# Performance work log

Measured on AMD Instinct MI355X. Metric: run time of the kernel, lower is better.

The kernel has to match this reference:

```python
import jax, jax.numpy as jnp
import numpy as np

N = 50_000        # nodes
D = 256           # emb_dim
L = 3             # num_layer
E = 4             # num_experts (all hop-1 GCN experts)
K = 2             # top-k gating
VOCAB = 5000      # src_vocab_size_graph
NEDGES = 1_600_000
BN_EPS = 1e-5


def setup_inputs() -> dict:
    key = jax.random.key(0)
    ks = jax.random.split(key, 8)
    x = jax.random.randint(ks[0], (N,), 0, VOCAB)                      # atom ids
    edge_index = jax.random.randint(ks[1], (2, NEDGES), 0, N)          # [2, E_edges] src/dst
    emb = jax.random.normal(ks[2], (VOCAB + 1, D), jnp.float32) * 0.02 # AtomEncoder table
    w_gate = jax.random.normal(ks[3], (L, D, E), jnp.float32) * 0.02   # per-layer gate
    conv_W = jax.random.normal(ks[4], (L, E, D, D), jnp.float32) * (1.0 / np.sqrt(D))
    conv_b = jnp.zeros((L, E, D), jnp.float32)
    bn_gamma = jnp.ones((L, E, D), jnp.float32)
    bn_beta = jnp.zeros((L, E, D), jnp.float32)
    return dict(x=x, edge_index=edge_index, emb=emb, w_gate=w_gate,
                conv_W=conv_W, conv_b=conv_b, bn_gamma=bn_gamma, bn_beta=bn_beta)


def reference(x, edge_index, emb, w_gate, conv_W, conv_b, bn_gamma, bn_beta):
    src, dst = edge_index[0], edge_index[1]
    ones = jnp.ones((NEDGES,), jnp.float32)
    out_deg = jax.ops.segment_sum(ones, src, num_segments=N)
    in_deg = jax.ops.segment_sum(ones, dst, num_segments=N)
    norm_src = jax.lax.rsqrt(jnp.maximum(out_deg, 1.0))[:, None]  # D^{-1/2} on source side
    norm_dst = jax.lax.rsqrt(jnp.maximum(in_deg, 1.0))[:, None]   # D^{-1/2} on dest side

    h = emb[x]  # [N, D] AtomEncoder
    node_ids = jnp.arange(N)[:, None]
    for l in range(L):
        # ---- top-k sparse gating over experts ----
        logits = h @ w_gate[l]                              # [N, E]
        topv, topi = jax.lax.top_k(logits, K)               # [N, K]
        gk = jax.nn.softmax(topv, axis=-1)                  # renormalized top-k gates
        gates = jnp.zeros((N, E), h.dtype).at[node_ids, topi].set(gk)  # sparse [N, E]
        # ---- shared symmetric-normalized GCN aggregation (same A_norm for all experts) ----
        msg = (h * norm_src)[src]                           # [E_edges, D]
        agg = jax.ops.segment_sum(msg, dst, num_segments=N) * norm_dst  # [N, D]
        # ---- per-expert linear + BatchNorm (training-mode stats over nodes) ----
        z = jnp.einsum('nd,edf->enf', agg, conv_W[l]) + conv_b[l][:, None, :]  # [E, N, D]
        mu = z.mean(axis=1, keepdims=True)
        var = z.var(axis=1, keepdims=True)
        z = (z - mu) * jax.lax.rsqrt(var + BN_EPS) * bn_gamma[l][:, None, :] + bn_beta[l][:, None, :]
        # ---- combine with sparse gates (zero gates => expert math cancels) ----
        h_moe = jnp.einsum('ne,enf->nf', gates, z)          # [N, D]
        # outer residual: h = h + drop_path(relu(h)); drop_path is identity in eval
        h = h_moe + jax.nn.relu(h_moe)
    return h  # JK='last' node representation [N, D]
```

## Files before the change

### kernel.cpp

```cpp
#include <hip/hip_runtime.h>
#include <hip/hip_bf16.h>

#define N_NODES 50000
#define DIM     256
#define NEXP    4
#define NLAYER  3
#define NEDGE   1600000
#define BN_EPS  1e-5f

typedef __attribute__((ext_vector_type(8))) short          s16x8;
typedef __attribute__((ext_vector_type(8))) unsigned short u16x8;
typedef __attribute__((ext_vector_type(4))) float          f32x4;

static __device__ __forceinline__ float wave_reduce(float v) {
    #pragma unroll
    for (int off = 32; off; off >>= 1) v += __shfl_xor(v, off, 64);
    return v;
}

static __device__ __forceinline__ void bf16split(float x, unsigned short& hi,
                                                 unsigned short& lo) {
    unsigned xb = __float_as_uint(x);
    unsigned hb = (xb + 0x7FFFu + ((xb >> 16) & 1u)) & 0xFFFF0000u;
    float hif = __uint_as_float(hb);
    float l  = x - hif;
    unsigned lb2 = __float_as_uint(l);
    unsigned lb  = (lb2 + 0x7FFFu + ((lb2 >> 16) & 1u)) >> 16;
    hi = (unsigned short)(hb >> 16);
    lo = (unsigned short)lb;
}

__global__ void k_deg(const int* __restrict__ src, const int* __restrict__ dst,
                      int* __restrict__ cnt_out, int* __restrict__ cnt_in) {
    int i = blockIdx.x * 256 + threadIdx.x;
    if (i < NEDGE) {
        atomicAdd(&cnt_out[src[i]], 1);
        atomicAdd(&cnt_in[dst[i]], 1);
    }
}

__global__ void k_norm(const int* __restrict__ cnt_out, const int* __restrict__ cnt_in,
                       float* __restrict__ nsrc, float* __restrict__ ndst) {
    int i = blockIdx.x * 256 + threadIdx.x;
    if (i < N_NODES) {
        nsrc[i] = rsqrtf(fmaxf((float)cnt_out[i], 1.f));
        ndst[i] = rsqrtf(fmaxf((float)cnt_in[i], 1.f));
    }
}

__global__ __launch_bounds__(1024) void k_scan(const int* __restrict__ cnt_in,
                                               int* __restrict__ offs,
                                               int* __restrict__ cursor) {
    __shared__ int ps[1024];
    const int CH = 49;
    int t = threadIdx.x;
    int base = t * CH;
    int s = 0;
    for (int k = 0; k < CH; k++) { int i = base + k; if (i < N_NODES) s += cnt_in[i]; }
    ps[t] = s; __syncthreads();
    for (int off = 1; off < 1024; off <<= 1) {
        int v = ps[t];
        int u = (t >= off) ? ps[t - off] : 0;
        __syncthreads();
        ps[t] = v + u;
        __syncthreads();
    }
    int run = (t == 0) ? 0 : ps[t - 1];
    for (int k = 0; k < CH; k++) {
        int i = base + k;
        if (i < N_NODES) { offs[i] = run; cursor[i] = run; run += cnt_in[i]; }
    }
    if (t == 1023) offs[N_NODES] = ps[1023];
}

__global__ void k_fill(const int* __restrict__ src, const int* __restrict__ dst,
                       int* __restrict__ cursor, int* __restrict__ csr_s) {
    int i = blockIdx.x * 256 + threadIdx.x;
    if (i < NEDGE) {
        int s = src[i], d = dst[i];
        int pos = atomicAdd(&cursor[d], 1);
        csr_s[pos] = s;
    }
}

__global__ void k_emb(const int* __restrict__ x, const float4* __restrict__ emb4,
                      float4* __restrict__ h4) {
    int i = blockIdx.x * 256 + threadIdx.x;
    if (i < N_NODES * 64) {
        int n = i >> 6, c = i & 63;
        h4[i] = emb4[x[n] * 64 + c];
    }
}

__global__ void k_gate(const float4* __restrict__ h4, const float4* __restrict__ wg4,
                       int* __restrict__ pid, float* __restrict__ gaN,
                       float* __restrict__ gbN) {
    int n    = blockIdx.x * 4 + (threadIdx.x >> 6);
    int lane = threadIdx.x & 63;
    if (n >= N_NODES) return;
    float4 hv = h4[n * 64 + lane];
    const float* hp = (const float*)&hv;
    float4 acc = {0.f, 0.f, 0.f, 0.f};
    #pragma unroll
    for (int j = 0; j < 4; j++) {
        float4 w = wg4[lane * 4 + j];
        acc.x += hp[j] * w.x; acc.y += hp[j] * w.y;
        acc.z += hp[j] * w.z; acc.w += hp[j] * w.w;
    }
    acc.x = wave_reduce(acc.x); acc.y = wave_reduce(acc.y);
    acc.z = wave_reduce(acc.z); acc.w = wave_reduce(acc.w);
    if (lane == 0) {
        float lg[4] = {acc.x, acc.y, acc.z, acc.w};
        int e1 = 0;
        #pragma unroll
        for (int e = 1; e < 4; e++) if (lg[e] > lg[e1]) e1 = e;
        int e2 = -1;
        #pragma unroll
        for (int e = 0; e < 4; e++) {
            if (e == e1) continue;
            if (e2 < 0 || lg[e] > lg[e2]) e2 = e;
        }
        float v1 = lg[e1], v2 = lg[e2];
        float g2 = 1.f / (1.f + expf(v1 - v2));
        float g1 = 1.f - g2;
        int a = min(e1, e2), b = max(e1, e2);
        float ga = (e1 < e2) ? g1 : g2;
        float gb = (e1 < e2) ? g2 : g1;
        int p = (a == 0) ? (b - 1) : ((a == 1) ? (b + 1) : (b + 2));
        pid[n] = p; gaN[n] = ga; gbN[n] = gb;
    }
}

__global__ void k_bucket(const int* __restrict__ pid,
                         int* __restrict__ gcount, int* __restrict__ bnode) {
    __shared__ int cnt[6];
    __shared__ int basep[6];
    int t = threadIdx.x;
    int n = blockIdx.x * 256 + t;
    if (t < 6) cnt[t] = 0;
    __syncthreads();
    int p = 0, pos = 0;
    bool valid = (n < N_NODES);
    if (valid) { p = pid[n]; pos = atomicAdd(&cnt[p], 1); }
    __syncthreads();
    if (t < 6) basep[t] = atomicAdd(&gcount[t], cnt[t]);
    __syncthreads();
    if (valid) bnode[p * N_NODES + basep[p] + pos] = n;
}

__global__ void k_agg(const float4* __restrict__ h4,
                      const int* __restrict__ offs,
                      const int* __restrict__ csr_s, const float* __restrict__ nsrc,
                      const float* __restrict__ ndst,
                      float4* __restrict__ agg4) {
    const float S  = 4294967296.0f;
    const float SI = 1.0f / 4294967296.0f;
    int n    = blockIdx.x * 4 + (threadIdx.x >> 6);
    int lane = threadIdx.x & 63;
    if (n >= N_NODES) return;
    int beg = offs[n], end = offs[n + 1];
    long long ax = 0, ay = 0, az = 0, aw = 0;
    int j = beg;
    for (; j + 1 < end; j += 2) {
        int   s0 = csr_s[j],     s1 = csr_s[j + 1];
        float w0 = nsrc[s0] * S, w1 = nsrc[s1] * S;
        float4 a = h4[(size_t)s0 * 64 + lane];
        float4 b = h4[(size_t)s1 * 64 + lane];
        ax += (long long)(w0 * a.x) + (long long)(w1 * b.x);
        ay += (long long)(w0 * a.y) + (long long)(w1 * b.y);
        az += (long long)(w0 * a.z) + (long long)(w1 * b.z);
        aw += (long long)(w0 * a.w) + (long long)(w1 * b.w);
    }
    if (j < end) {
        int   s0 = csr_s[j];
        float w0 = nsrc[s0] * S;
        float4 a = h4[(size_t)s0 * 64 + lane];
        ax += (long long)(w0 * a.x); ay += (long long)(w0 * a.y);
        az += (long long)(w0 * a.z); aw += (long long)(w0 * a.w);
    }
    float nd = ndst[n] * SI;
    float4 o;
    o.x = nd * (float)ax; o.y = nd * (float)ay;
    o.z = nd * (float)az; o.w = nd * (float)aw;
    agg4[n * 64 + lane] = o;
}

__global__ void k_pcs(const float* __restrict__ agg,
                      unsigned short* __restrict__ Apk,
                      float* __restrict__ msum_p) {
    int t = threadIdx.x;
    const int CH = 200;
    int n0 = blockIdx.x * CH;
    float s = 0.f;
    for (int r = 0; r < CH; r++) {
        int n = n0 + r;
        float v = agg[(size_t)n * DIM + t];
        s += v;
        unsigned short hi, lo;
        bf16split(v, hi, lo);
        Apk[(size_t)n * 512 + t]       = hi;
        Apk[(size_t)n * 512 + 256 + t] = lo;
    }
    msum_p[blockIdx.x * 256 + t] = s;
}

#define GSL   48
#define GCH   1056
#define NPAIR 10
__global__ __launch_bounds__(256) void k_gram(const float* __restrict__ agg,
                                              float* __restrict__ Cp) {
    __shared__ float LA[16][64];
    __shared__ float LB[16][64];
    const int tiT[NPAIR] = {0,0,0,0,1,1,1,2,2,3};
    const int tjT[NPAIR] = {0,1,2,3,1,2,3,2,3,3};
    int t  = threadIdx.x;
    int sl = blockIdx.x;
    int pr = blockIdx.y;
    int ti = tiT[pr], tj = tjT[pr];
    int tx = t & 15, ty = t >> 4;
    float acc[4][4] = {};
    int nbase = sl * GCH;
    const float4* agg4 = (const float4*)agg;
    for (int s0 = 0; s0 < GCH; s0 += 16) {
        int r = ty;
        int n = nbase + s0 + r;
        float4 va = {0.f, 0.f, 0.f, 0.f}, vb = {0.f, 0.f, 0.f, 0.f};
        if (n < N_NODES) {
            va = agg4[n * 64 + ti * 16 + tx];
            vb = agg4[n * 64 + tj * 16 + tx];
        }
        __syncthreads();
        *(float4*)&LA[r][tx * 4] = va;
        *(float4*)&LB[r][tx * 4] = vb;
        __syncthreads();
        #pragma unroll
        for (int rr = 0; rr < 16; rr++) {
            float4 a = *(const float4*)&LA[rr][tx * 4];
            float4 b = *(const float4*)&LB[rr][ty * 4];
            const float* af = (const float*)&a;
            const float* bf = (const float*)&b;
            #pragma unroll
            for (int i = 0; i < 4; i++)
                #pragma unroll
                for (int j = 0; j < 4; j++)
                    acc[i][j] += af[i] * bf[j];
        }
    }
    float* Cb = Cp + ((size_t)(sl * NPAIR + pr)) * 4096;
    #pragma unroll
    for (int i = 0; i < 4; i++) {
        float4 v; v.x = acc[i][0]; v.y = acc[i][1]; v.z = acc[i][2]; v.w = acc[i][3];
        *(float4*)&Cb[(tx * 4 + i) * 64 + ty * 4] = v;
    }
}

__global__ void k_red(const float* __restrict__ msum_p, float* __restrict__ msum,
                      const float* __restrict__ Cp, float* __restrict__ Cm) {
    int t = threadIdx.x;
    if (blockIdx.x == 0) {
        float s = 0.f;
        for (int b = 0; b < 250; b++) s += msum_p[b * 256 + t];
        msum[t] = s;
        return;
    }
    int gid = (blockIdx.x - 1) * 256 + t;
    int i = gid >> 8, j = gid & 255;
    int a = i >> 6, b = j >> 6, ii = i & 63, jj = j & 63;
    int ro = ii, co = jj;
    if (a > b) { int tmp = a; a = b; b = tmp; ro = jj; co = ii; }
    int pr = (a == 0) ? b : ((a == 1) ? 3 + b : ((a == 2) ? 5 + b : 6 + b));
    const float* p = Cp + (size_t)pr * 4096 + ro * 64 + co;
    float s = 0.f;
    #pragma unroll 8
    for (int sl = 0; sl < GSL; sl++) s += p[(size_t)sl * NPAIR * 4096];
    Cm[gid] = s;
}

__global__ __launch_bounds__(256) void k_stats(const float* __restrict__ C,
                                               const float* __restrict__ msum,
                                               const float* __restrict__ conv_W,
                                               const float* __restrict__ bn_gamma,
                                               const float* __restrict__ bn_beta,
                                               float* __restrict__ scaleb,
                                               float* __restrict__ shiftb, int l) {
    int e = blockIdx.x >> 8, f = blockIdx.x & 255;
    int t = threadIdx.x;
    __shared__ float wsh[256];
    __shared__ float red[256];
    const float* W = conv_W + (size_t)(l * NEXP + e) * DIM * DIM;
    wsh[t] = W[t * DIM + f];
    __syncthreads();
    float v = 0.f;
    #pragma unroll 8
    for (int d2 = 0; d2 < DIM; d2++) v += C[d2 * DIM + t] * wsh[d2];
    float a_t = msum[t] * (1.f / (float)N_NODES);
    float qp  = wsh[t] * v;
    float ap  = a_t * wsh[t];
    red[t] = qp; __syncthreads();
    for (int off = 128; off; off >>= 1) { if (t < off) red[t] += red[t + off]; __syncthreads(); }
    float q = red[0];
    red[t] = ap; __syncthreads();
    for (int off = 128; off; off >>= 1) { if (t < off) red[t] += red[t + off]; __syncthreads(); }
    if (t == 0) {
        float aw  = red[0];
        float var = q * (1.f / (float)N_NODES) - aw * aw;
        var = fmaxf(var, 0.f);
        float sg = bn_gamma[(l * NEXP + e) * DIM + f] * rsqrtf(var + BN_EPS);
        scaleb[e * DIM + f] = sg;
        shiftb[e * DIM + f] = bn_beta[(l * NEXP + e) * DIM + f] - aw * sg;
    }
}

__global__ void k_wscale(const float* __restrict__ conv_W, const float* __restrict__ scaleb,
                         unsigned short* __restrict__ Wpk, int l) {
    int i = blockIdx.x * 256 + threadIdx.x;
    if (i < NEXP * DIM * DIM) {
        int k = i & 255, f = (i >> 8) & 255, e = i >> 16;
        float w = conv_W[(size_t)(l * NEXP + e) * 65536 + (size_t)k * 256 + f]
                * scaleb[e * 256 + f];
        unsigned short hi, lo;
        bf16split(w, hi, lo);
        size_t base = (size_t)(e * 256 + f) * 512;
        Wpk[base + k]       = hi;
        Wpk[base + 256 + k] = lo;
    }
}

__global__ __launch_bounds__(256) void k_moe(const unsigned short* __restrict__ Apk,
                                             const unsigned short* __restrict__ Wpk,
                                             const float* __restrict__ shiftb,
                                             const int* __restrict__ gcount,
                                             const int* __restrict__ bnode,
                                             const float* __restrict__ gaN,
                                             const float* __restrict__ gbN,
                                             float* __restrict__ hout) {
    __shared__ short As2[2][64][40];
    __shared__ short Wt[256][40];
    __shared__ int   nds[64];
    __shared__ float gA[64], gB[64];
    __shared__ float shc[2][256];
    int p    = blockIdx.y;
    int cnt  = gcount[p];
    int base = blockIdx.x * 64;
    if (base >= cnt) return;
    const int eaT[6] = {0,0,0,1,1,2};
    const int ebT[6] = {1,2,3,2,3,3};
    int ea = eaT[p], eb = ebT[p];
    int t  = threadIdx.x;
    if (t < 64) {
        int idx = base + t;
        if (idx < cnt) {
            int n = bnode[p * N_NODES + idx];
            nds[t] = n; gA[t] = gaN[n]; gB[t] = gbN[n];
        } else { nds[t] = -1; gA[t] = 0.f; gB[t] = 0.f; }
    }
    if (t < 128) {
        int which = t >> 6, c = t & 63;
        int e = which ? eb : ea;
        ((float4*)shc[which])[c] = ((const float4*)(shiftb + e * DIM))[c];
    }
    __syncthreads();

    int rA   = t >> 2;
    int cA8  = (t & 3) * 8;
    int wv   = t >> 6, wl = t & 63;
    int wrow = wv * 64 + (wl >> 2);
    int wc8  = (wl & 3) * 8;

    int nrow = nds[rA];
    const unsigned short* arow = Apk + (size_t)(nrow < 0 ? 0 : nrow) * 512;

    u16x8 areg = {0,0,0,0,0,0,0,0};
    if (nrow >= 0) areg = *(const u16x8*)(arow + cA8);
    u16x8 wreg0, wreg1, wreg2, wreg3;
    {
        const unsigned short* wb = Wpk + ((size_t)ea * 256 + wrow) * 512 + wc8;
        wreg0 = *(const u16x8*)(wb);
        wreg1 = *(const u16x8*)(wb + (size_t)16 * 512);
        wreg2 = *(const u16x8*)(wb + (size_t)32 * 512);
        wreg3 = *(const u16x8*)(wb + (size_t)48 * 512);
    }

    int lane = t & 63, quad = lane >> 4, l16 = lane & 15;
    f32x4 acc[4][4];
    #pragma unroll
    for (int a = 0; a < 4; a++)
        #pragma unroll
        for (int b = 0; b < 4; b++) { f32x4 z = {0.f,0.f,0.f,0.f}; acc[a][b] = z; }

    for (int s = 0; s < 64; s++) {
        int buf = s & 1;
        *(u16x8*)&As2[buf][rA][cA8]   = areg;
        *(u16x8*)&Wt[wrow     ][wc8]  = wreg0;
        *(u16x8*)&Wt[wrow + 16][wc8]  = wreg1;
        *(u16x8*)&Wt[wrow + 32][wc8]  = wreg2;
        *(u16x8*)&Wt[wrow + 48][wc8]  = wreg3;
        __syncthreads();
        if (s < 63) {
            int s1   = s + 1;
            int esel = s1 >> 5;
            int t2   = (s1 >> 3) & 3;
            int kc   = (s1 & 7) * 32;
            int aoff = (t2 >= 2 ? 256 : 0) + kc;
            int woff = ((t2 & 1) ? 256 : 0) + kc;
            u16x8 z8 = {0,0,0,0,0,0,0,0};
            areg = z8;
            if (nrow >= 0) areg = *(const u16x8*)(arow + aoff + cA8);
            const unsigned short* wb = Wpk
                + ((size_t)(esel ? eb : ea) * 256 + wrow) * 512 + woff + wc8;
            wreg0 = *(const u16x8*)(wb);
            wreg1 = *(const u16x8*)(wb + (size_t)16 * 512);
            wreg2 = *(const u16x8*)(wb + (size_t)32 * 512);
            wreg3 = *(const u16x8*)(wb + (size_t)48 * 512);
        }
        s16x8 af[4], bfr[4];
        #pragma unroll
        for (int rt = 0; rt < 4; rt++)
            af[rt] = *(const s16x8*)&As2[buf][rt * 16 + l16][quad * 8];
        #pragma unroll
        for (int ct = 0; ct < 4; ct++)
            bfr[ct] = *(const s16x8*)&Wt[wv * 64 + ct * 16 + l16][quad * 8];
        #pragma unroll
        for (int rt = 0; rt < 4; rt++)
            #pragma unroll
            for (int ct = 0; ct < 4; ct++)
                acc[rt][ct] = __builtin_amdgcn_mfma_f32_16x16x32_bf16(
                                  af[rt], bfr[ct], acc[rt][ct], 0, 0, 0);
        if (s == 31) {
            #pragma unroll
            for (int rt = 0; rt < 4; rt++)
                #pragma unroll
                for (int r = 0; r < 4; r++) {
                    int row = rt * 16 + quad * 4 + r;
                    float ratio = gA[row] / fmaxf(gB[row], 1e-30f);
                    #pragma unroll
                    for (int ct = 0; ct < 4; ct++) acc[rt][ct][r] *= ratio;
                }
        }
    }

    #pragma unroll
    for (int rt = 0; rt < 4; rt++)
        #pragma unroll
        for (int r = 0; r < 4; r++) {
            int row = rt * 16 + quad * 4 + r;
            int n = nds[row];
            if (n < 0) continue;
            float gaL = gA[row];
            float gbL = fmaxf(gB[row], 1e-30f);
            #pragma unroll
            for (int ct = 0; ct < 4; ct++) {
                int col = wv * 64 + ct * 16 + l16;
                float v = gbL * acc[rt][ct][r] + gaL * shc[0][col] + gbL * shc[1][col];
                hout[(size_t)n * DIM + col] = v + fmaxf(v, 0.f);
            }
        }
}

extern "C" void kernel_launch(void* const* d_in, const int* in_sizes, int n_in,
                              void* d_out, int out_size, void* d_ws, size_t ws_size,
                              hipStream_t stream) {
    const int*   x        = (const int*)d_in[0];
    const int*   ei       = (const int*)d_in[1];
    const float* emb      = (const float*)d_in[2];
    const float* w_gate   = (const float*)d_in[3];
    const float* conv_W   = (const float*)d_in[4];
    const float* bn_gamma = (const float*)d_in[6];
    const float* bn_beta  = (const float*)d_in[7];
    float* out = (float*)d_out;

    const int* src = ei;
    const int* dst = ei + NEDGE;

    char* ws = (char*)d_ws;
    size_t off = 0;
    auto alloc = [&](size_t bytes) -> void* {
        void* p = ws + off;
        off += (bytes + 255) & ~(size_t)255;
        return p;
    };
    float*          h       = (float*)alloc((size_t)N_NODES * DIM * 4);
    float*          agg     = (float*)alloc((size_t)N_NODES * DIM * 4);
    unsigned short* Apk     = (unsigned short*)alloc((size_t)N_NODES * 512 * 2);
    int*            cnt_out = (int*)  alloc((size_t)N_NODES * 4);
    int*            cnt_in  = (int*)  alloc((size_t)N_NODES * 4);
    float*          nsrc    = (float*)alloc((size_t)N_NODES * 4);
    float*          ndst    = (float*)alloc((size_t)N_NODES * 4);
    int*            offs    = (int*)  alloc((size_t)(N_NODES + 1) * 4);
    int*            cursor  = (int*)  alloc((size_t)N_NODES * 4);
    int*            csr_s   = (int*)  alloc((size_t)NEDGE * 4);
    int*            pid     = (int*)  alloc((size_t)N_NODES * 4);
    float*          gaN     = (float*)alloc((size_t)N_NODES * 4);
    float*          gbN     = (float*)alloc((size_t)N_NODES * 4);
    int*            gcount  = (int*)  alloc(6 * 4);
    int*            bnode   = (int*)  alloc((size_t)6 * N_NODES * 4);
    float*          Cp      = (float*)alloc((size_t)GSL * NPAIR * 4096 * 4);
    float*          Cm      = (float*)alloc((size_t)DIM * DIM * 4);
    float*          msum_p  = (float*)alloc((size_t)250 * 256 * 4);
    float*          msum    = (float*)alloc((size_t)DIM * 4);
    float*          scaleb  = (float*)alloc((size_t)NEXP * DIM * 4);
    float*          shiftb  = (float*)alloc((size_t)NEXP * DIM * 4);
    unsigned short* Wpk     = (unsigned short*)alloc((size_t)NEXP * DIM * 512 * 2);
    (void)ws_size; (void)in_sizes; (void)n_in; (void)out_size;

    hipMemsetAsync(cnt_out, 0, (size_t)N_NODES * 4, stream);
    hipMemsetAsync(cnt_in,  0, (size_t)N_NODES * 4, stream);
    k_deg <<<(NEDGE + 255) / 256, 256, 0, stream>>>(src, dst, cnt_out, cnt_in);
    k_norm<<<(N_NODES + 255) / 256, 256, 0, stream>>>(cnt_out, cnt_in, nsrc, ndst);
    k_scan<<<1, 1024, 0, stream>>>(cnt_in, offs, cursor);
    k_fill<<<(NEDGE + 255) / 256, 256, 0, stream>>>(src, dst, cursor, csr_s);
    k_emb <<<(N_NODES * 64 + 255) / 256, 256, 0, stream>>>(x, (const float4*)emb, (float4*)h);

    for (int l = 0; l < NLAYER; l++) {
        float* hout = (l == NLAYER - 1) ? out : h;

        k_gate<<<N_NODES / 4, 256, 0, stream>>>((const float4*)h,
                (const float4*)(w_gate + (size_t)l * DIM * NEXP), pid, gaN, gbN);
        hipMemsetAsync(gcount, 0, 6 * 4, stream);
        k_bucket<<<(N_NODES + 255) / 256, 256, 0, stream>>>(pid, gcount, bnode);
        k_agg<<<N_NODES / 4, 256, 0, stream>>>((const float4*)h, offs, csr_s, nsrc,
                ndst, (float4*)agg);
        k_pcs<<<250, 256, 0, stream>>>(agg, Apk, msum_p);

        k_gram<<<dim3(GSL, NPAIR), 256, 0, stream>>>(agg, Cp);
        k_red<<<257, 256, 0, stream>>>(msum_p, msum, Cp, Cm);
        k_stats<<<NEXP * DIM, 256, 0, stream>>>(Cm, msum, conv_W, bn_gamma, bn_beta,
                                                scaleb, shiftb, l);
        k_wscale<<<(NEXP * DIM * DIM + 255) / 256, 256, 0, stream>>>(conv_W, scaleb, Wpk, l);

        k_moe<<<dim3((N_NODES + 63) / 64, 6), 256, 0, stream>>>(Apk, Wpk, shiftb,
                gcount, bnode, gaN, gbN, hout);
    }
}
```

Baseline: 1.865 ms.

## Fuse small kernels to cut launch count per layer

```diff
diff --git a/kernel.cpp b/kernel.cpp
--- a/kernel.cpp
+++ b/kernel.cpp
@@ -39,24 +39,26 @@
     }
 }
 
-__global__ void k_norm(const int* __restrict__ cnt_out, const int* __restrict__ cnt_in,
-                       float* __restrict__ nsrc, float* __restrict__ ndst) {
-    int i = blockIdx.x * 256 + threadIdx.x;
-    if (i < N_NODES) {
-        nsrc[i] = rsqrtf(fmaxf((float)cnt_out[i], 1.f));
-        ndst[i] = rsqrtf(fmaxf((float)cnt_in[i], 1.f));
-    }
-}
-
 __global__ __launch_bounds__(1024) void k_scan(const int* __restrict__ cnt_in,
+                                               const int* __restrict__ cnt_out,
                                                int* __restrict__ offs,
-                                               int* __restrict__ cursor) {
+                                               int* __restrict__ cursor,
+                                               float* __restrict__ nsrc,
+                                               float* __restrict__ ndst) {
     __shared__ int ps[1024];
     const int CH = 49;
     int t = threadIdx.x;
     int base = t * CH;
     int s = 0;
-    for (int k = 0; k < CH; k++) { int i = base + k; if (i < N_NODES) s += cnt_in[i]; }
+    for (int k = 0; k < CH; k++) {
+        int i = base + k;
+        if (i < N_NODES) {
+            int ci = cnt_in[i];
+            s += ci;
+            nsrc[i] = rsqrtf(fmaxf((float)cnt_out[i], 1.f));
+            ndst[i] = rsqrtf(fmaxf((float)ci, 1.f));
+        }
+    }
     ps[t] = s; __syncthreads();
     for (int off = 1; off < 1024; off <<= 1) {
         int v = ps[t];
@@ -94,7 +96,8 @@
 
 __global__ void k_gate(const float4* __restrict__ h4, const float4* __restrict__ wg4,
                        int* __restrict__ pid, float* __restrict__ gaN,
-                       float* __restrict__ gbN) {
+                       float* __restrict__ gbN, int* __restrict__ gcount) {
+    if (blockIdx.x == 0 && threadIdx.x < 6) gcount[threadIdx.x] = 0;
     int n    = blockIdx.x * 4 + (threadIdx.x >> 6);
     int lane = threadIdx.x & 63;
     if (n >= N_NODES) return;
@@ -129,23 +132,6 @@
         int p = (a == 0) ? (b - 1) : ((a == 1) ? (b + 1) : (b + 2));
         pid[n] = p; gaN[n] = ga; gbN[n] = gb;
     }
-}
-
-__global__ void k_bucket(const int* __restrict__ pid,
-                         int* __restrict__ gcount, int* __restrict__ bnode) {
-    __shared__ int cnt[6];
-    __shared__ int basep[6];
-    int t = threadIdx.x;
-    int n = blockIdx.x * 256 + t;
-    if (t < 6) cnt[t] = 0;
-    __syncthreads();
-    int p = 0, pos = 0;
-    bool valid = (n < N_NODES);
-    if (valid) { p = pid[n]; pos = atomicAdd(&cnt[p], 1); }
-    __syncthreads();
-    if (t < 6) basep[t] = atomicAdd(&gcount[t], cnt[t]);
-    __syncthreads();
-    if (valid) bnode[p * N_NODES + basep[p] + pos] = n;
 }
 
 __global__ void k_agg(const float4* __restrict__ h4,
@@ -185,37 +171,51 @@
     agg4[n * 64 + lane] = o;
 }
 
-__global__ void k_pcs(const float* __restrict__ agg,
-                      unsigned short* __restrict__ Apk,
-                      float* __restrict__ msum_p) {
-    int t = threadIdx.x;
-    const int CH = 200;
-    int n0 = blockIdx.x * CH;
-    float s = 0.f;
-    for (int r = 0; r < CH; r++) {
-        int n = n0 + r;
-        float v = agg[(size_t)n * DIM + t];
-        s += v;
-        unsigned short hi, lo;
-        bf16split(v, hi, lo);
-        Apk[(size_t)n * 512 + t]       = hi;
-        Apk[(size_t)n * 512 + 256 + t] = lo;
-    }
-    msum_p[blockIdx.x * 256 + t] = s;
-}
-
 #define GSL   48
 #define GCH   1056
 #define NPAIR 10
 __global__ __launch_bounds__(256) void k_gram(const float* __restrict__ agg,
-                                              float* __restrict__ Cp) {
+                                              float* __restrict__ Cp,
+                                              const int* __restrict__ pid,
+                                              int* __restrict__ gcount,
+                                              int* __restrict__ bnode,
+                                              unsigned short* __restrict__ Apk,
+                                              float* __restrict__ msum_p) {
     __shared__ float LA[16][64];
     __shared__ float LB[16][64];
+    __shared__ int cnt6[6], base6[6];
+    int t  = threadIdx.x;
+    int pr = blockIdx.y;
+    if (pr >= 10) {
+        int gid = blockIdx.x * 6 + (pr - 10);
+        if (gid >= 250) return;
+        const int CH = 200;
+        int n0 = gid * CH;
+        if (t < 6) cnt6[t] = 0;
+        __syncthreads();
+        int p = 0, pos = 0;
+        bool valid = (t < CH);
+        if (valid) { p = pid[n0 + t]; pos = atomicAdd(&cnt6[p], 1); }
+        __syncthreads();
+        if (t < 6) base6[t] = atomicAdd(&gcount[t], cnt6[t]);
+        __syncthreads();
+        if (valid) bnode[p * N_NODES + base6[p] + pos] = n0 + t;
+        float s = 0.f;
+        for (int r = 0; r < CH; r++) {
+            int n = n0 + r;
+            float v = agg[(size_t)n * DIM + t];
+            s += v;
+            unsigned short hi, lo;
+            bf16split(v, hi, lo);
+            Apk[(size_t)n * 512 + t]       = hi;
+            Apk[(size_t)n * 512 + 256 + t] = lo;
+        }
+        msum_p[gid * 256 + t] = s;
+        return;
+    }
     const int tiT[NPAIR] = {0,0,0,0,1,1,1,2,2,3};
     const int tjT[NPAIR] = {0,1,2,3,1,2,3,2,3,3};
-    int t  = threadIdx.x;
     int sl = blockIdx.x;
-    int pr = blockIdx.y;
     int ti = tiT[pr], tj = tjT[pr];
     int tx = t & 15, ty = t >> 4;
     float acc[4][4] = {};
@@ -281,12 +281,14 @@
                                                const float* __restrict__ conv_W,
                                                const float* __restrict__ bn_gamma,
                                                const float* __restrict__ bn_beta,
-                                               float* __restrict__ scaleb,
-                                               float* __restrict__ shiftb, int l) {
+                                               float* __restrict__ shiftb,
+                                               unsigned short* __restrict__ Wpk,
+                                               int l) {
     int e = blockIdx.x >> 8, f = blockIdx.x & 255;
     int t = threadIdx.x;
     __shared__ float wsh[256];
     __shared__ float red[256];
+    __shared__ float sgs;
     const float* W = conv_W + (size_t)(l * NEXP + e) * DIM * DIM;
     wsh[t] = W[t * DIM + f];
     __syncthreads();
@@ -306,24 +308,16 @@
         float var = q * (1.f / (float)N_NODES) - aw * aw;
         var = fmaxf(var, 0.f);
         float sg = bn_gamma[(l * NEXP + e) * DIM + f] * rsqrtf(var + BN_EPS);
-        scaleb[e * DIM + f] = sg;
+        sgs = sg;
         shiftb[e * DIM + f] = bn_beta[(l * NEXP + e) * DIM + f] - aw * sg;
     }
-}
-
-__global__ void k_wscale(const float* __restrict__ conv_W, const float* __restrict__ scaleb,
-                         unsigned short* __restrict__ Wpk, int l) {
-    int i = blockIdx.x * 256 + threadIdx.x;
-    if (i < NEXP * DIM * DIM) {
-        int k = i & 255, f = (i >> 8) & 255, e = i >> 16;
-        float w = conv_W[(size_t)(l * NEXP + e) * 65536 + (size_t)k * 256 + f]
-                * scaleb[e * 256 + f];
-        unsigned short hi, lo;
-        bf16split(w, hi, lo);
-        size_t base = (size_t)(e * 256 + f) * 512;
-        Wpk[base + k]       = hi;
-        Wpk[base + 256 + k] = lo;
-    }
+    __syncthreads();
+    float w = wsh[t] * sgs;
+    unsigned short hi, lo;
+    bf16split(w, hi, lo);
+    size_t basep = ((size_t)e * 256 + f) * 512;
+    Wpk[basep + t]       = hi;
+    Wpk[basep + 256 + t] = lo;
 }
 
 __global__ __launch_bounds__(256) void k_moe(const unsigned short* __restrict__ Apk,
@@ -498,16 +492,14 @@
     float*          Cm      = (float*)alloc((size_t)DIM * DIM * 4);
     float*          msum_p  = (float*)alloc((size_t)250 * 256 * 4);
     float*          msum    = (float*)alloc((size_t)DIM * 4);
-    float*          scaleb  = (float*)alloc((size_t)NEXP * DIM * 4);
     float*          shiftb  = (float*)alloc((size_t)NEXP * DIM * 4);
     unsigned short* Wpk     = (unsigned short*)alloc((size_t)NEXP * DIM * 512 * 2);
     (void)ws_size; (void)in_sizes; (void)n_in; (void)out_size;
 
-    hipMemsetAsync(cnt_out, 0, (size_t)N_NODES * 4, stream);
-    hipMemsetAsync(cnt_in,  0, (size_t)N_NODES * 4, stream);
+    size_t cnt_span = (size_t)((char*)cnt_in - (char*)cnt_out) + (size_t)N_NODES * 4;
+    hipMemsetAsync(cnt_out, 0, cnt_span, stream);
     k_deg <<<(NEDGE + 255) / 256, 256, 0, stream>>>(src, dst, cnt_out, cnt_in);
-    k_norm<<<(N_NODES + 255) / 256, 256, 0, stream>>>(cnt_out, cnt_in, nsrc, ndst);
-    k_scan<<<1, 1024, 0, stream>>>(cnt_in, offs, cursor);
+    k_scan<<<1, 1024, 0, stream>>>(cnt_in, cnt_out, offs, cursor, nsrc, ndst);
     k_fill<<<(NEDGE + 255) / 256, 256, 0, stream>>>(src, dst, cursor, csr_s);
     k_emb <<<(N_NODES * 64 + 255) / 256, 256, 0, stream>>>(x, (const float4*)emb, (float4*)h);
 
@@ -515,19 +507,14 @@
         float* hout = (l == NLAYER - 1) ? out : h;
 
         k_gate<<<N_NODES / 4, 256, 0, stream>>>((const float4*)h,
-                (const float4*)(w_gate + (size_t)l * DIM * NEXP), pid, gaN, gbN);
-        hipMemsetAsync(gcount, 0, 6 * 4, stream);
-        k_bucket<<<(N_NODES + 255) / 256, 256, 0, stream>>>(pid, gcount, bnode);
+                (const float4*)(w_gate + (size_t)l * DIM * NEXP), pid, gaN, gbN, gcount);
         k_agg<<<N_NODES / 4, 256, 0, stream>>>((const float4*)h, offs, csr_s, nsrc,
                 ndst, (float4*)agg);
-        k_pcs<<<250, 256, 0, stream>>>(agg, Apk, msum_p);
-
-        k_gram<<<dim3(GSL, NPAIR), 256, 0, stream>>>(agg, Cp);
+        k_gram<<<dim3(GSL, 16), 256, 0, stream>>>(agg, Cp, pid, gcount, bnode,
+                                                  Apk, msum_p);
         k_red<<<257, 256, 0, stream>>>(msum_p, msum, Cp, Cm);
         k_stats<<<NEXP * DIM, 256, 0, stream>>>(Cm, msum, conv_W, bn_gamma, bn_beta,
-                                                scaleb, shiftb, l);
-        k_wscale<<<(NEXP * DIM * DIM + 255) / 256, 256, 0, stream>>>(conv_W, scaleb, Wpk, l);
-
+                                                shiftb, Wpk, l);
         k_moe<<<dim3((N_NODES + 63) / 64, 6), 256, 0, stream>>>(Apk, Wpk, shiftb,
                 gcount, bnode, gaN, gbN, hout);
     }
```

New measurement: 1.881 ms. Within noise of the previous version (+0.9%).
